# Kernel tuning notes

Measured on AMD Instinct MI355X. Metric: run time of the kernel, lower is better.

## Reference

```python
import jax, jax.numpy as jnp
import numpy as np

DISTANCE_W = 1.0
ANGLE_W = 1.0
EPS = 1e-12  # matches F.normalize eps


def setup_inputs() -> dict:
    key = jax.random.key(0)
    k1, k2 = jax.random.split(key)
    student_emb = jax.random.normal(k1, (1024, 512), dtype=jnp.float32)
    teacher_emb = jax.random.normal(k2, (1024, 512), dtype=jnp.float32)
    return {"student_emb": student_emb, "teacher_emb": teacher_emb}


def _pairwise_similarity(emb):
    # F.normalize(emb, dim=1) then emb @ emb.T -> [N, N] cosine similarity
    norm = jnp.maximum(jnp.linalg.norm(emb, axis=1, keepdims=True), EPS)
    en = emb / norm
    return en @ en.T


def _angle_similarity(emb):
    # ||e_i - e_j||^2 for all pairs, computed via the GEMM expansion
    # (same math as the N x N x D broadcast in the original, no O(N^2 D) tensor)
    sq = jnp.sum(emb * emb, axis=1)  # [N]
    gram = emb @ emb.T               # [N, N]
    return sq[:, None] + sq[None, :] - 2.0 * gram


def reference(student_emb, teacher_emb):
    loss_dist = jnp.mean((_pairwise_similarity(student_emb) - _pairwise_similarity(teacher_emb)) ** 2)
    loss_angle = jnp.mean((_angle_similarity(student_emb) - _angle_similarity(teacher_emb)) ** 2)
    return DISTANCE_W * loss_dist + ANGLE_W * loss_angle
```

## Files before the change

### kernel.cpp

```cpp
#include <hip/hip_runtime.h>

typedef short short8 __attribute__((ext_vector_type(8)));
typedef float f32x16 __attribute__((ext_vector_type(16)));
typedef unsigned short ushort;

#define DD 512


__device__ __forceinline__ short to_bf16(float f) {
    unsigned int u = __float_as_uint(f);
    u += 0x7FFFu + ((u >> 16) & 1u);
    return (short)(u >> 16);
}

__device__ __forceinline__ short8 pack8(float4 a, float4 b) {
    short8 r;
    r[0] = to_bf16(a.x); r[1] = to_bf16(a.y); r[2] = to_bf16(a.z); r[3] = to_bf16(a.w);
    r[4] = to_bf16(b.x); r[5] = to_bf16(b.y); r[6] = to_bf16(b.z); r[7] = to_bf16(b.w);
    return r;
}

__device__ __forceinline__ float dot4(float4 v) {
    return v.x*v.x + v.y*v.y + v.z*v.z + v.w*v.w;
}

__global__ __launch_bounds__(256) void convert_kernel(const float* __restrict__ S,
                                                      const float* __restrict__ T,
                                                      ushort* __restrict__ bf,
                                                      float* __restrict__ sqarr,
                                                      float* __restrict__ accw) {
    const int t    = threadIdx.x;
    const int lane = t & 63;
    const int row  = blockIdx.x * 4 + (t >> 6);
    const float* src = (row < 1024) ? (S + (size_t)row * DD)
                                    : (T + (size_t)(row - 1024) * DD);
    float4 v0 = ((const float4*)src)[lane * 2];
    float4 v1 = ((const float4*)src)[lane * 2 + 1];
    *(short8*)(bf + (size_t)row * DD + lane * 8) = pack8(v0, v1);
    float s = dot4(v0) + dot4(v1);
    #pragma unroll
    for (int off = 32; off > 0; off >>= 1) s += __shfl_down(s, off);
    if (lane == 0) {
        sqarr[row]        = s;
        sqarr[2048 + row] = 1.0f / fmaxf(sqrtf(s), 1e-12f);
    }
    if (blockIdx.x == 0 && t < 17) ((unsigned int*)(accw))[t] = 0u;
}

__global__ __launch_bounds__(256) void rkd_tile_kernel(const ushort* __restrict__ bf,
                                                       const float* __restrict__ sqarr,
                                                       float* __restrict__ accw,
                                                       float* __restrict__ out) {
    __shared__ ushort tiles[2][16384];
    __shared__ float statI[4][64];
    __shared__ float statJ[4][64];
    __shared__ float wsum[4];

    const int t = threadIdx.x;
    const int I = (blockIdx.x >> 4) * 64;
    const int J = (blockIdx.x & 15) * 64;
    const int w = t >> 6;
    const int L = t & 63;
    const int c = L & 31;
    const int h = L >> 5;
    const int rowsel = (w & 1) * 32;
    const int colsel = (w >> 1) * 32;

    const ushort* bS = bf;
    const ushort* bT = bf + (size_t)1024 * DD;

    {
        const int a = t >> 6, r = t & 63;
        const int so = a * 1024;
        statI[a][r] = sqarr[so + I + r];
        statJ[a][r] = sqarr[so + J + r];
    }

    const int lrow  = L >> 3;
    const int lchk  = (L & 7) ^ lrow;
    const int lgoff = lrow * DD + lchk * 8;

    const ushort* gtab[8];
    int loff[8];
    #pragma unroll
    for (int j = 0; j < 8; ++j) {
        const int q   = w * 8 + j;
        const int ts  = q >> 3;
        const int sub = q & 7;
        const ushort* gmat = (ts == 0 || ts == 2) ? bS : bT;
        const int gbase = (ts < 2) ? I : J;
        gtab[j] = gmat + (size_t)(gbase + sub * 8) * DD + lgoff;
        loff[j] = ts * 4096 + sub * 512;
    }

    f32x16 accS, accT;
    #pragma unroll
    for (int i2 = 0; i2 < 16; ++i2) { accS[i2] = 0.0f; accT[i2] = 0.0f; }

    #pragma unroll
    for (int j = 0; j < 8; ++j)
        __builtin_amdgcn_global_load_lds(
            (const __attribute__((address_space(1))) void*)(gtab[j]),
            (__attribute__((address_space(3))) void*)(&tiles[0][0] + loff[j]), 16, 0, 0);

    for (int i = 0; i < 8; ++i) {
        __syncthreads();
        if (i < 7) {
            const int k0 = (i + 1) * 64;
            ushort* nb = &tiles[(i + 1) & 1][0];
            #pragma unroll
            for (int j = 0; j < 8; ++j)
                __builtin_amdgcn_global_load_lds(
                    (const __attribute__((address_space(1))) void*)(gtab[j] + k0),
                    (__attribute__((address_space(3))) void*)(nb + loff[j]), 16, 0, 0);
        }
        const ushort* base = &tiles[i & 1][0];
        #pragma unroll
        for (int step = 0; step < 4; ++step) {
            const int us = ((step * 2 + h) ^ (c & 7)) * 8;
            short8 afS = *(const short8*)(base + (rowsel + c) * 64 + us);
            short8 afT = *(const short8*)(base + 4096 + (rowsel + c) * 64 + us);
            short8 bfS = *(const short8*)(base + 8192 + (colsel + c) * 64 + us);
            short8 bfT = *(const short8*)(base + 12288 + (colsel + c) * 64 + us);
            accS = __builtin_amdgcn_mfma_f32_32x32x16_bf16(afS, bfS, accS, 0, 0, 0);
            accT = __builtin_amdgcn_mfma_f32_32x32x16_bf16(afT, bfT, accT, 0, 0, 0);
        }
    }

    const int colg = colsel + c;
    const float js  = statJ[0][colg], jt  = statJ[1][colg];
    const float rjs = statJ[2][colg], rjt = statJ[3][colg];

    float local = 0.0f;
    #pragma unroll
    for (int reg = 0; reg < 16; ++reg) {
        const int rowg = rowsel + (reg & 3) + 8 * (reg >> 2) + 4 * h;
        float is  = statI[0][rowg], it  = statI[1][rowg];
        float ris = statI[2][rowg], rit = statI[3][rowg];
        float gs = accS[reg], gt = accT[reg];
        float d1 = gs * ris * rjs - gt * rit * rjt;
        float d2 = (is + js - 2.0f * gs) - (it + jt - 2.0f * gt);
        local += d1 * d1 + d2 * d2;
    }

    #pragma unroll
    for (int off = 32; off > 0; off >>= 1) local += __shfl_down(local, off);
    if (L == 0) wsum[w] = local;
    __syncthreads();

    if (t == 0) {
        float blk = wsum[0] + wsum[1] + wsum[2] + wsum[3];
        atomicAdd(&accw[blockIdx.x & 15], blk);
        __threadfence();
        unsigned int old = atomicAdd((unsigned int*)(accw + 16), 1u);
        if (old == 255u) {
            __threadfence();
            float tot = 0.0f;
            #pragma unroll
            for (int s2 = 0; s2 < 16; ++s2)
                tot += __hip_atomic_load(&accw[s2], __ATOMIC_RELAXED, __HIP_MEMORY_SCOPE_AGENT);
            out[0] = tot * (1.0f / 1048576.0f);
        }
    }
}

extern "C" void kernel_launch(void* const* d_in, const int* in_sizes, int n_in,
                              void* d_out, int out_size, void* d_ws, size_t ws_size,
                              hipStream_t stream) {
    const float* S = (const float*)d_in[0];
    const float* T = (const float*)d_in[1];
    ushort* bf   = (ushort*)d_ws;
    float* sqarr = (float*)((char*)d_ws + 2 * 1024 * 1024);
    float* accw  = sqarr + 4096;
    float* out   = (float*)d_out;

    convert_kernel<<<512, 256, 0, stream>>>(S, T, bf, sqarr, accw);
    rkd_tile_kernel<<<256, 256, 0, stream>>>(bf, sqarr, accw, out);
}
```

Measured before the change: 72.72 us.

## Exploit Gram symmetry: compute only upper-triangle tiles with doubled off-diagonal weight

Remaps the grid to cover only the upper-triangular 32x64 tiles of the N x N similarity matrices, weighting strictly upper entries by 2 and the diagonal by 1. Blocks shrink to two waves with 32-row A tiles, and the grid has 272 blocks. This roughly halves MFMA work and reduces global/LDS traffic. In exchange it adds a small per-block loop for index decoding, gives an uneven block count relative to CU count, and uses smaller blocks with less reuse per tile.

```diff
diff --git a/kernel.cpp b/kernel.cpp
--- a/kernel.cpp
+++ b/kernel.cpp
@@ -47,50 +47,55 @@
     if (blockIdx.x == 0 && t < 17) ((unsigned int*)(accw))[t] = 0u;
 }
 
-__global__ __launch_bounds__(256) void rkd_tile_kernel(const ushort* __restrict__ bf,
+__global__ __launch_bounds__(128) void rkd_tile_kernel(const ushort* __restrict__ bf,
                                                        const float* __restrict__ sqarr,
                                                        float* __restrict__ accw,
                                                        float* __restrict__ out) {
-    __shared__ ushort tiles[2][16384];
-    __shared__ float statI[4][64];
+    __shared__ ushort tiles[2][12288];
+    __shared__ float statI[4][32];
     __shared__ float statJ[4][64];
-    __shared__ float wsum[4];
+    __shared__ float wsum[2];
 
     const int t = threadIdx.x;
-    const int I = (blockIdx.x >> 4) * 64;
-    const int J = (blockIdx.x & 15) * 64;
+
+    int rem = blockIdx.x, a = 0;
+    for (;;) { int cnt = 16 - (a >> 1); if (rem < cnt) break; rem -= cnt; ++a; }
+    const int b2 = (a >> 1) + rem;
+    const int I = a * 32;
+    const int J = b2 * 64;
+
     const int w = t >> 6;
     const int L = t & 63;
     const int c = L & 31;
     const int h = L >> 5;
-    const int rowsel = (w & 1) * 32;
-    const int colsel = (w >> 1) * 32;
+    const int colsel = w * 32;
 
     const ushort* bS = bf;
     const ushort* bT = bf + (size_t)1024 * DD;
 
     {
-        const int a = t >> 6, r = t & 63;
-        const int so = a * 1024;
-        statI[a][r] = sqarr[so + I + r];
-        statJ[a][r] = sqarr[so + J + r];
+        const int a2 = t >> 5, r = t & 31;
+        statI[a2][r]      = sqarr[a2 * 1024 + I + r];
+        statJ[a2][r]      = sqarr[a2 * 1024 + J + r];
+        statJ[a2][32 + r] = sqarr[a2 * 1024 + J + 32 + r];
     }
 
     const int lrow  = L >> 3;
     const int lchk  = (L & 7) ^ lrow;
     const int lgoff = lrow * DD + lchk * 8;
 
-    const ushort* gtab[8];
-    int loff[8];
+    const ushort* gtab[12];
+    int loff[12];
     #pragma unroll
-    for (int j = 0; j < 8; ++j) {
-        const int q   = w * 8 + j;
-        const int ts  = q >> 3;
-        const int sub = q & 7;
-        const ushort* gmat = (ts == 0 || ts == 2) ? bS : bT;
-        const int gbase = (ts < 2) ? I : J;
+    for (int j = 0; j < 12; ++j) {
+        const int q = w * 12 + j;
+        const ushort* gmat; int gbase, lo, sub;
+        if (q < 4)       { gmat = bS; gbase = I; sub = q;      lo = 0    + sub * 512; }
+        else if (q < 8)  { gmat = bT; gbase = I; sub = q - 4;  lo = 2048 + sub * 512; }
+        else if (q < 16) { gmat = bS; gbase = J; sub = q - 8;  lo = 4096 + sub * 512; }
+        else             { gmat = bT; gbase = J; sub = q - 16; lo = 8192 + sub * 512; }
         gtab[j] = gmat + (size_t)(gbase + sub * 8) * DD + lgoff;
-        loff[j] = ts * 4096 + sub * 512;
+        loff[j] = lo;
     }
 
     f32x16 accS, accT;
@@ -98,7 +103,7 @@
     for (int i2 = 0; i2 < 16; ++i2) { accS[i2] = 0.0f; accT[i2] = 0.0f; }
 
     #pragma unroll
-    for (int j = 0; j < 8; ++j)
+    for (int j = 0; j < 12; ++j)
         __builtin_amdgcn_global_load_lds(
             (const __attribute__((address_space(1))) void*)(gtab[j]),
             (__attribute__((address_space(3))) void*)(&tiles[0][0] + loff[j]), 16, 0, 0);
@@ -109,7 +114,7 @@
             const int k0 = (i + 1) * 64;
             ushort* nb = &tiles[(i + 1) & 1][0];
             #pragma unroll
-            for (int j = 0; j < 8; ++j)
+            for (int j = 0; j < 12; ++j)
                 __builtin_amdgcn_global_load_lds(
                     (const __attribute__((address_space(1))) void*)(gtab[j] + k0),
                     (__attribute__((address_space(3))) void*)(nb + loff[j]), 16, 0, 0);
@@ -118,29 +123,32 @@
         #pragma unroll
         for (int step = 0; step < 4; ++step) {
             const int us = ((step * 2 + h) ^ (c & 7)) * 8;
-            short8 afS = *(const short8*)(base + (rowsel + c) * 64 + us);
-            short8 afT = *(const short8*)(base + 4096 + (rowsel + c) * 64 + us);
-            short8 bfS = *(const short8*)(base + 8192 + (colsel + c) * 64 + us);
-            short8 bfT = *(const short8*)(base + 12288 + (colsel + c) * 64 + us);
-            accS = __builtin_amdgcn_mfma_f32_32x32x16_bf16(afS, bfS, accS, 0, 0, 0);
-            accT = __builtin_amdgcn_mfma_f32_32x32x16_bf16(afT, bfT, accT, 0, 0, 0);
+            short8 afS = *(const short8*)(base + c * 64 + us);
+            short8 afT = *(const short8*)(base + 2048 + c * 64 + us);
+            short8 bS8 = *(const short8*)(base + 4096 + (colsel + c) * 64 + us);
+            short8 bT8 = *(const short8*)(base + 8192 + (colsel + c) * 64 + us);
+            accS = __builtin_amdgcn_mfma_f32_32x32x16_bf16(afS, bS8, accS, 0, 0, 0);
+            accT = __builtin_amdgcn_mfma_f32_32x32x16_bf16(afT, bT8, accT, 0, 0, 0);
         }
     }
 
     const int colg = colsel + c;
+    const int jg   = J + colg;
     const float js  = statJ[0][colg], jt  = statJ[1][colg];
     const float rjs = statJ[2][colg], rjt = statJ[3][colg];
 
     float local = 0.0f;
     #pragma unroll
     for (int reg = 0; reg < 16; ++reg) {
-        const int rowg = rowsel + (reg & 3) + 8 * (reg >> 2) + 4 * h;
+        const int rowg = (reg & 3) + 8 * (reg >> 2) + 4 * h;
+        const int ig = I + rowg;
+        float wgt = (jg > ig) ? 2.0f : ((jg == ig) ? 1.0f : 0.0f);
         float is  = statI[0][rowg], it  = statI[1][rowg];
         float ris = statI[2][rowg], rit = statI[3][rowg];
         float gs = accS[reg], gt = accT[reg];
         float d1 = gs * ris * rjs - gt * rit * rjt;
         float d2 = (is + js - 2.0f * gs) - (it + jt - 2.0f * gt);
-        local += d1 * d1 + d2 * d2;
+        local += wgt * (d1 * d1 + d2 * d2);
     }
 
     #pragma unroll
@@ -149,11 +157,11 @@
     __syncthreads();
 
     if (t == 0) {
-        float blk = wsum[0] + wsum[1] + wsum[2] + wsum[3];
+        float blk = wsum[0] + wsum[1];
         atomicAdd(&accw[blockIdx.x & 15], blk);
         __threadfence();
         unsigned int old = atomicAdd((unsigned int*)(accw + 16), 1u);
-        if (old == 255u) {
+        if (old == 271u) {
             __threadfence();
             float tot = 0.0f;
             #pragma unroll
@@ -175,5 +183,5 @@
     float* out   = (float*)d_out;
 
     convert_kernel<<<512, 256, 0, stream>>>(S, T, bf, sqarr, accw);
-    rkd_tile_kernel<<<256, 256, 0, stream>>>(bf, sqarr, accw, out);
+    rkd_tile_kernel<<<272, 128, 0, stream>>>(bf, sqarr, accw, out);
 }
```

After: 71.94 us. About the same (-1.1%).
